# Performance work log

Measured on AMD Instinct MI355X. Metric: run time of the kernel, lower is better.

## Reference

```python
import jax, jax.numpy as jnp
import numpy as np

D_MODEL, D_K, D_V, D_H, SEQ = 1024, 64, 64, 16, 4096


def setup_inputs() -> dict:
    key = jax.random.key(0)
    ks = jax.random.split(key, 16)
    s = lambda fan_in: 1.0 / np.sqrt(fan_in)
    return {
        "X": jax.random.normal(ks[0], (SEQ, D_MODEL), jnp.float32),
        # shared Q/K/V projections (nn.Linear stores weight as [out, in])
        "Wq": jax.random.uniform(ks[1], (D_K, D_MODEL), jnp.float32, -s(D_MODEL), s(D_MODEL)),
        "bq": jax.random.uniform(ks[2], (D_K,), jnp.float32, -s(D_MODEL), s(D_MODEL)),
        "Wk": jax.random.uniform(ks[3], (D_K, D_MODEL), jnp.float32, -s(D_MODEL), s(D_MODEL)),
        "bk": jax.random.uniform(ks[4], (D_K,), jnp.float32, -s(D_MODEL), s(D_MODEL)),
        "Wv": jax.random.uniform(ks[5], (D_V, D_MODEL), jnp.float32, -s(D_MODEL), s(D_MODEL)),
        "bv": jax.random.uniform(ks[6], (D_V,), jnp.float32, -s(D_MODEL), s(D_MODEL)),
        # per-head linears stacked along head axis
        "Whq": jax.random.uniform(ks[7], (D_H, D_K, D_K), jnp.float32, -s(D_K), s(D_K)),
        "bhq": jax.random.uniform(ks[8], (D_H, D_K), jnp.float32, -s(D_K), s(D_K)),
        "Whk": jax.random.uniform(ks[9], (D_H, D_K, D_K), jnp.float32, -s(D_K), s(D_K)),
        "bhk": jax.random.uniform(ks[10], (D_H, D_K), jnp.float32, -s(D_K), s(D_K)),
        "Whv": jax.random.uniform(ks[11], (D_H, D_V, D_V), jnp.float32, -s(D_V), s(D_V)),
        "bhv": jax.random.uniform(ks[12], (D_H, D_V), jnp.float32, -s(D_V), s(D_V)),
        # final projection: d_h*d_v -> d_model
        "Wo": jax.random.uniform(ks[13], (D_MODEL, D_H * D_V), jnp.float32, -s(D_H * D_V), s(D_H * D_V)),
        "bo": jax.random.uniform(ks[14], (D_MODEL,), jnp.float32, -s(D_H * D_V), s(D_H * D_V)),
    }


def reference(X, Wq, bq, Wk, bk, Wv, bv, Whq, bhq, Whk, bhk, Whv, bhv, Wo, bo):
    # shared projections: [T, d_k] / [T, d_v]
    Q = X @ Wq.T + bq
    K = X @ Wk.T + bk
    V = X @ Wv.T + bv
    # per-head linears, all heads at once: [H, T, d_k]
    qh = jnp.einsum("tk,hjk->htj", Q, Whq) + bhq[:, None, :]
    kh = jnp.einsum("tk,hjk->htj", K, Whk) + bhk[:, None, :]
    vh = jnp.einsum("tv,hjv->htj", V, Whv) + bhv[:, None, :]
    # scaled dot-product attention per head: [H, T, T]
    scale = 1.0 / jnp.sqrt(jnp.asarray(Q.shape[-1], X.dtype))
    attn = jax.nn.softmax(jnp.einsum("htk,hsk->hts", qh, kh) * scale, axis=-1)
    rep = jnp.einsum("hts,hsv->htv", attn, vh)  # [H, T, d_v]
    # hstack heads -> [T, H*d_v], then final projection
    concat = rep.transpose(1, 0, 2).reshape(X.shape[0], -1)
    return concat @ Wo.T + bo
```

## Files before the change

### kernel.cpp

```cpp
#include <hip/hip_runtime.h>

#define T 4096
#define DM 1024
#define DK 64
#define H 16

typedef short s8 __attribute__((ext_vector_type(8)));
typedef float f4 __attribute__((ext_vector_type(4)));
typedef float f16v __attribute__((ext_vector_type(16)));
typedef unsigned short us4 __attribute__((ext_vector_type(4)));
typedef unsigned u32x2 __attribute__((ext_vector_type(2)));
typedef unsigned u32x4 __attribute__((ext_vector_type(4)));
typedef __bf16 bf2 __attribute__((ext_vector_type(2)));

#define MFMA16(a,b,c) __builtin_amdgcn_mfma_f32_16x16x32_bf16((a),(b),(c),0,0,0)
#define MFMA32(a,b,c) __builtin_amdgcn_mfma_f32_32x32x16_bf16((a),(b),(c),0,0,0)
#define SCALE_Q 0.18033688011112042f

__device__ __forceinline__ unsigned short f2bf(float x){
  __bf16 b = (__bf16)x;
  return __builtin_bit_cast(unsigned short, b);
}
__device__ __forceinline__ unsigned pk2(float a, float b){
  bf2 v; v[0] = (__bf16)a; v[1] = (__bf16)b;
  return __builtin_bit_cast(unsigned, v);
}

__device__ __forceinline__ void gload16(const void* g, void* lds){
  __builtin_amdgcn_global_load_lds((const __attribute__((address_space(1))) unsigned int*)g,
                                   (__attribute__((address_space(3))) unsigned int*)lds,
                                   16, 0, 0);
}

__device__ __forceinline__ void swp(unsigned X, unsigned Y, unsigned &E, unsigned &O){
#if __has_builtin(__builtin_amdgcn_permlane32_swap)
  auto a = __builtin_amdgcn_permlane32_swap(X, Y, false, false);
  E = a[0]; O = a[1];
#else
  int l = threadIdx.x & 63;
  unsigned sx = __builtin_amdgcn_ds_bpermute(((l & 31) << 2), X);
  unsigned sy = __builtin_amdgcn_ds_bpermute(((l & 31) << 2), Y);
  unsigned hx = __builtin_amdgcn_ds_bpermute((((l & 31) + 32) << 2), X);
  unsigned hy = __builtin_amdgcn_ds_bpermute((((l & 31) + 32) << 2), Y);
  E = (l < 32) ? sx : sy;
  O = (l < 32) ? hx : hy;
#endif
}

__global__ void cvt_bf16(const float* __restrict__ in, unsigned short* __restrict__ out, int n4){
  int i = blockIdx.x * blockDim.x + threadIdx.x;
  if (i >= n4) return;
  float4 v = reinterpret_cast<const float4*>(in)[i];
  us4 o;
  o[0] = f2bf(v.x); o[1] = f2bf(v.y); o[2] = f2bf(v.z); o[3] = f2bf(v.w);
  reinterpret_cast<us4*>(out)[i] = o;
}

#define N_WOB (DM * DM / 4)
#define N_W3  (64 * DM / 4)
#define N_WH  (16 * 64 * 64 / 4)
__global__ __launch_bounds__(256) void prep_all(
    const float* __restrict__ Wo,
    const float* __restrict__ Wq, const float* __restrict__ Wk, const float* __restrict__ Wv,
    const float* __restrict__ Whq, const float* __restrict__ Whk, const float* __restrict__ Whv,
    const float* __restrict__ bq, const float* __restrict__ bk, const float* __restrict__ bv,
    const float* __restrict__ bhq, const float* __restrict__ bhk, const float* __restrict__ bhv,
    unsigned short* __restrict__ Wob, unsigned short* __restrict__ W3b,
    unsigned short* __restrict__ Whb, float* __restrict__ beff){
  int idx = blockIdx.x * 256 + threadIdx.x;
  if (idx < N_WOB){
    float4 v = reinterpret_cast<const float4*>(Wo)[idx];
    us4 o; o[0]=f2bf(v.x); o[1]=f2bf(v.y); o[2]=f2bf(v.z); o[3]=f2bf(v.w);
    reinterpret_cast<us4*>(Wob)[idx] = o;
    return;
  }
  idx -= N_WOB;
  if (idx < 3 * N_W3){
    int seg = idx / N_W3, i = idx - seg * N_W3;
    const float* src = (seg == 0) ? Wq : ((seg == 1) ? Wk : Wv);
    float4 v = reinterpret_cast<const float4*>(src)[i];
    us4 o; o[0]=f2bf(v.x); o[1]=f2bf(v.y); o[2]=f2bf(v.z); o[3]=f2bf(v.w);
    reinterpret_cast<us4*>(W3b)[seg * N_W3 + i] = o;
    return;
  }
  idx -= 3 * N_W3;
  if (idx < 3 * N_WH){
    int seg = idx / N_WH, i = idx - seg * N_WH;
    const float* src = (seg == 0) ? Whq : ((seg == 1) ? Whk : Whv);
    float s = (seg == 0) ? SCALE_Q : 1.0f;
    float4 v = reinterpret_cast<const float4*>(src)[i];
    us4 o; o[0]=f2bf(v.x*s); o[1]=f2bf(v.y*s); o[2]=f2bf(v.z*s); o[3]=f2bf(v.w*s);
    reinterpret_cast<us4*>(Whb)[seg * N_WH + i] = o;
    return;
  }
  idx -= 3 * N_WH;
  if (idx < 3072){
    int seg = idx >> 10, j = idx & 1023;
    const float* Wh = (seg == 0) ? Whq : ((seg == 1) ? Whk : Whv);
    const float* b  = (seg == 0) ? bq  : ((seg == 1) ? bk  : bv);
    const float* bh = (seg == 0) ? bhq : ((seg == 1) ? bhk : bhv);
    float s = (seg == 0) ? SCALE_Q : 1.0f;
    const float* wr = Wh + j * 64;
    float acc = 0.f;
    #pragma unroll 8
    for (int k = 0; k < 64; ++k) acc += wr[k] * b[k];
    beff[idx] = (acc + bh[j]) * s;
  }
}

template<int MODE, int BM, int BN, int NT>
__global__ __launch_bounds__(256) void gemmX(const unsigned short* __restrict__ A,
                       const unsigned short* __restrict__ B,
                       const float* __restrict__ bias,
                       unsigned short* __restrict__ q_out,
                       unsigned short* __restrict__ k_out,
                       unsigned short* __restrict__ v_out,
                       float* __restrict__ f_out){
  __shared__ __align__(16) short la[2][BM * 64];
  __shared__ __align__(16) short lb[2][BN * 64];
  const int tid = threadIdx.x;
  const int wv = tid >> 6, l = tid & 63;
  const int lr = l & 15, lh = l >> 4;
  const int wr = wv >> 1, wc = wv & 1;
  const int tm = blockIdx.x / NT, tn = blockIdx.x % NT;
  const int t0 = tm * BM, o0 = tn * BN;
  constexpr int MF = BM / 32;
  constexpr int NF = BN / 32;
  constexpr int ACH = BM / 32;
  constexpr int BCH = BN / 32;
  constexpr int LAB = BM * 128;
  constexpr int LBB = BN * 128;

  f4 acc[MF][NF];
  #pragma unroll
  for (int i = 0; i < MF; ++i)
    #pragma unroll
    for (int j = 0; j < NF; ++j) acc[i][j] = (f4){0.f, 0.f, 0.f, 0.f};

  const int srow = tid >> 3;
  const int scs  = (tid & 7) ^ (srow & 7);
  const unsigned short* ap = A + (size_t)(t0 + srow) * DM + scs * 8;
  const unsigned short* bp = B + (size_t)(o0 + srow) * DM + scs * 8;
  char* ad = (char*)&la[0][0] + tid * 16;
  char* bd = (char*)&lb[0][0] + tid * 16;

  auto stage = [&](int BUF){
    #pragma unroll
    for (int i = 0; i < ACH; ++i)
      gload16(ap + (size_t)i * 32 * DM, ad + BUF * LAB + i * 4096);
    #pragma unroll
    for (int i = 0; i < BCH; ++i)
      gload16(bp + (size_t)i * 32 * DM, bd + BUF * LBB + i * 4096);
    ap += 64; bp += 64;
  };

  const int asw0 = (lh ^ (lr & 7)) * 16, asw1 = ((lh ^ 4) ^ (lr & 7)) * 16;
  const char* aB0 = (const char*)&la[0][0] + (wr * (BM / 2) + lr) * 128 + asw0;
  const char* aB1 = (const char*)&la[0][0] + (wr * (BM / 2) + lr) * 128 + asw1;
  const char* bB0 = (const char*)&lb[0][0] + (wc * (BN / 2) + lr) * 128 + asw0;
  const char* bB1 = (const char*)&lb[0][0] + (wc * (BN / 2) + lr) * 128 + asw1;

  auto step = [&](int BUF, bool dostage){
    if (dostage) stage(BUF ^ 1);
    s8 af[MF][2], bfr[NF][2];
    #pragma unroll
    for (int mf = 0; mf < MF; ++mf){
      af[mf][0] = *(const s8*)(aB0 + BUF * LAB + mf * 2048);
      af[mf][1] = *(const s8*)(aB1 + BUF * LAB + mf * 2048);
    }
    #pragma unroll
    for (int nf = 0; nf < NF; ++nf){
      bfr[nf][0] = *(const s8*)(bB0 + BUF * LBB + nf * 2048);
      bfr[nf][1] = *(const s8*)(bB1 + BUF * LBB + nf * 2048);
    }
    __builtin_amdgcn_s_setprio(1);
    #pragma unroll
    for (int mf = 0; mf < MF; ++mf)
      #pragma unroll
      for (int nf = 0; nf < NF; ++nf){
        acc[mf][nf] = MFMA16(af[mf][0], bfr[nf][0], acc[mf][nf]);
        acc[mf][nf] = MFMA16(af[mf][1], bfr[nf][1], acc[mf][nf]);
      }
    __builtin_amdgcn_s_setprio(0);
    __syncthreads();
  };

  stage(0);
  __syncthreads();
  #pragma unroll 1
  for (int t2 = 0; t2 < 8; ++t2){
    step(0, true);
    step(1, t2 < 7);
  }

  #pragma unroll
  for (int nf = 0; nf < NF; ++nf){
    int o = o0 + wc * (BN / 2) + nf * 16 + lr;
    float bs = (MODE == 4) ? 0.f : bias[o];
    int sel = o >> 6, oc = o & 63;
    unsigned short* yo = (sel == 0) ? q_out : ((sel == 1) ? k_out : v_out);
    #pragma unroll
    for (int mf = 0; mf < MF; ++mf)
      #pragma unroll
      for (int r = 0; r < 4; ++r){
        int t = t0 + wr * (BM / 2) + mf * 16 + lh * 4 + r;
        float v = acc[mf][nf][r] + bs;
        if (MODE == 2) f_out[(size_t)t * DM + o] = v;
        else           yo[(size_t)t * 64 + oc] = f2bf(v);
      }
  }
}

__global__ __launch_bounds__(256) void gemm_heads(const unsigned short* __restrict__ Yq,
                        const unsigned short* __restrict__ Yk,
                        const unsigned short* __restrict__ Yv,
                        const unsigned short* __restrict__ Whb,
                        const float* __restrict__ beff,
                        unsigned short* __restrict__ qhb,
                        unsigned short* __restrict__ khb,
                        unsigned short* __restrict__ vtb){
  const int tid = threadIdx.x;
  const int wv = tid >> 6, l = tid & 63;
  const int lr = l & 15, lh = l >> 4;
  const int rem = blockIdx.x % 48, tb = blockIdx.x / 48;
  const int kind = rem >> 4, h = rem & 15;
  const unsigned short* Y = (kind == 0) ? Yq : ((kind == 1) ? Yk : Yv);
  const unsigned short* B = Whb + (size_t)rem * 4096;
  const int t0 = tb * 256 + wv * 64;

  s8 wf[4][2], yf[4][2];
  #pragma unroll
  for (int nf = 0; nf < 4; ++nf)
    #pragma unroll
    for (int hf = 0; hf < 2; ++hf)
      wf[nf][hf] = *reinterpret_cast<const s8*>(B + (size_t)(nf * 16 + lr) * 64 + hf * 32 + lh * 8);
  #pragma unroll
  for (int mf = 0; mf < 4; ++mf)
    #pragma unroll
    for (int hf = 0; hf < 2; ++hf)
      yf[mf][hf] = *reinterpret_cast<const s8*>(Y + (size_t)(t0 + mf * 16 + lr) * 64 + hf * 32 + lh * 8);

  f4 acc[4][4];
  #pragma unroll
  for (int i = 0; i < 4; ++i)
    #pragma unroll
    for (int j = 0; j < 4; ++j) acc[i][j] = (f4){0.f, 0.f, 0.f, 0.f};

  if (kind < 2){
    #pragma unroll
    for (int mf = 0; mf < 4; ++mf)
      #pragma unroll
      for (int nf = 0; nf < 4; ++nf){
        acc[mf][nf] = MFMA16(yf[mf][0], wf[nf][0], acc[mf][nf]);
        acc[mf][nf] = MFMA16(yf[mf][1], wf[nf][1], acc[mf][nf]);
      }
    unsigned short* out = (kind == 0) ? qhb : khb;
    #pragma unroll
    for (int nf = 0; nf < 4; ++nf){
      int j = nf * 16 + lr;
      float bs = beff[rem * 64 + j];
      #pragma unroll
      for (int mf = 0; mf < 4; ++mf)
        #pragma unroll
        for (int r = 0; r < 4; ++r){
          int t = t0 + mf * 16 + lh * 4 + r;
          out[((size_t)h * T + t) * DK + j] = f2bf(acc[mf][nf][r] + bs);
        }
    }
  } else {
    #pragma unroll
    for (int nf = 0; nf < 4; ++nf)
      #pragma unroll
      for (int mf = 0; mf < 4; ++mf){
        acc[nf][mf] = MFMA16(wf[nf][0], yf[mf][0], acc[nf][mf]);
        acc[nf][mf] = MFMA16(wf[nf][1], yf[mf][1], acc[nf][mf]);
      }
    #pragma unroll
    for (int nf = 0; nf < 4; ++nf){
      float4 bsv = *reinterpret_cast<const float4*>(beff + rem * 64 + nf * 16 + lh * 4);
      #pragma unroll
      for (int r = 0; r < 4; ++r){
        int j = nf * 16 + lh * 4 + r;
        float bs = (r == 0) ? bsv.x : ((r == 1) ? bsv.y : ((r == 2) ? bsv.z : bsv.w));
        #pragma unroll
        for (int mf = 0; mf < 4; ++mf){
          int t = t0 + mf * 16 + lr;
          vtb[((size_t)h * DK + j) * T + t] = f2bf(acc[nf][mf][r] + bs);
        }
      }
    }
  }
}

__global__ __launch_bounds__(128) void attn_fwd(const unsigned short* __restrict__ qh,
                         const unsigned short* __restrict__ kh,
                         const unsigned short* __restrict__ vt,
                         unsigned short* __restrict__ cat){
  __shared__ __align__(16) char ldsb[2][16384];
  const int tid = threadIdx.x;
  const int wv = tid >> 6, l = tid & 63;
  const int l31 = l & 31, h5 = l >> 5, l7 = l & 7;
  const int h = blockIdx.x >> 5, qblk = blockIdx.x & 31;
  const int Qw = qblk * 128 + wv * 64;

  s8 qf[2][4];
  #pragma unroll
  for (int qt = 0; qt < 2; ++qt)
    #pragma unroll
    for (int kk = 0; kk < 4; ++kk)
      qf[qt][kk] = *reinterpret_cast<const s8*>(
          qh + ((size_t)h * T + Qw + qt * 32 + l31) * DK + kk * 16 + h5 * 8);

  float ls[2] = {0.f, 0.f};
  f16v oa[2][2];
  #pragma unroll
  for (int qt = 0; qt < 2; ++qt)
    #pragma unroll
    for (int dt = 0; dt < 2; ++dt)
      #pragma unroll
      for (int i = 0; i < 16; ++i) oa[qt][dt][i] = 0.f;

  const int srow = tid >> 3;
  const int scs  = (tid & 7) ^ (srow & 7);
  const unsigned short* kp = kh + (size_t)h * T * DK + srow * DK + scs * 8;
  const unsigned short* vp = vt + (size_t)h * DK * T + srow * T + scs * 8;
  char* sd = &ldsb[0][0] + tid * 16;

  auto stage = [&](int BUF){
    #pragma unroll
    for (int i = 0; i < 4; ++i)
      gload16(kp + (size_t)i * 16 * DK, sd + BUF * 16384 + i * 2048);
    #pragma unroll
    for (int i = 0; i < 4; ++i)
      gload16(vp + (size_t)i * 16 * T, sd + BUF * 16384 + 8192 + i * 2048);
    kp += 64 * DK; vp += 64;
  };

  const char* ba[4];
  #pragma unroll
  for (int kk = 0; kk < 4; ++kk)
    ba[kk] = &ldsb[0][0] + l31 * 128 + ((((kk << 1) | h5) ^ l7) << 4);

  auto step = [&](int BUF, bool dostage){
    if (dostage) stage(BUF ^ 1);
    const int bo = BUF * 16384;
    s8 kf0[4], kf1[4], vf0[4], vf1[4];
    #pragma unroll
    for (int kk = 0; kk < 4; ++kk){
      kf0[kk] = *(const s8*)(ba[kk] + bo);
      kf1[kk] = *(const s8*)(ba[kk] + bo + 4096);
    }
    #pragma unroll
    for (int p = 0; p < 4; ++p){
      vf0[p] = *(const s8*)(ba[p] + bo + 8192);
      vf1[p] = *(const s8*)(ba[p] + bo + 12288);
    }
    #pragma unroll
    for (int qt = 0; qt < 2; ++qt){
      f16v sc0, sc1;
      #pragma unroll
      for (int i = 0; i < 16; ++i){ sc0[i] = 0.f; sc1[i] = 0.f; }
      __builtin_amdgcn_s_setprio(1);
      #pragma unroll
      for (int kk = 0; kk < 4; ++kk) sc0 = MFMA32(kf0[kk], qf[qt][kk], sc0);
      #pragma unroll
      for (int kk = 0; kk < 4; ++kk) sc1 = MFMA32(kf1[kk], qf[qt][kk], sc1);
      __builtin_amdgcn_s_setprio(0);
      float p0[16], p1[16];
      #pragma unroll
      for (int i = 0; i < 16; ++i){
        p0[i] = __builtin_amdgcn_exp2f(sc0[i]);
        p1[i] = __builtin_amdgcn_exp2f(sc1[i]);
      }
      float r0 = (p0[0]+p0[1]) + (p0[2]+p0[3]);
      float r1 = (p0[4]+p0[5]) + (p0[6]+p0[7]);
      float r2 = (p0[8]+p0[9]) + (p0[10]+p0[11]);
      float r3 = (p0[12]+p0[13]) + (p0[14]+p0[15]);
      float r4 = (p1[0]+p1[1]) + (p1[2]+p1[3]);
      float r5 = (p1[4]+p1[5]) + (p1[6]+p1[7]);
      float r6 = (p1[8]+p1[9]) + (p1[10]+p1[11]);
      float r7 = (p1[12]+p1[13]) + (p1[14]+p1[15]);
      ls[qt] += ((r0+r1)+(r2+r3)) + ((r4+r5)+(r6+r7));
      unsigned a0 = pk2(p0[0],p0[1]),  a1 = pk2(p0[2],p0[3]);
      unsigned a2 = pk2(p0[4],p0[5]),  a3 = pk2(p0[6],p0[7]);
      unsigned a4 = pk2(p0[8],p0[9]),  a5 = pk2(p0[10],p0[11]);
      unsigned a6 = pk2(p0[12],p0[13]), a7 = pk2(p0[14],p0[15]);
      unsigned b0 = pk2(p1[0],p1[1]),  b1 = pk2(p1[2],p1[3]);
      unsigned b2 = pk2(p1[4],p1[5]),  b3 = pk2(p1[6],p1[7]);
      unsigned b4 = pk2(p1[8],p1[9]),  b5 = pk2(p1[10],p1[11]);
      unsigned b6 = pk2(p1[12],p1[13]), b7 = pk2(p1[14],p1[15]);
      unsigned e0,o0, e1,o1, e2,o2, e3,o3, e4,o4, e5,o5, e6,o6, e7,o7;
      swp(a0, a2, e0, o0);  swp(a1, a3, e1, o1);
      swp(a4, a6, e2, o2);  swp(a5, a7, e3, o3);
      swp(b0, b2, e4, o4);  swp(b1, b3, e5, o5);
      swp(b4, b6, e6, o6);  swp(b5, b7, e7, o7);
      u32x4 pu0 = {e0, e1, o0, o1};
      u32x4 pu1 = {e2, e3, o2, o3};
      u32x4 pu2 = {e4, e5, o4, o5};
      u32x4 pu3 = {e6, e7, o6, o7};
      s8 pa0 = __builtin_bit_cast(s8, pu0);
      s8 pa1 = __builtin_bit_cast(s8, pu1);
      s8 pa2 = __builtin_bit_cast(s8, pu2);
      s8 pa3 = __builtin_bit_cast(s8, pu3);
      __builtin_amdgcn_s_setprio(1);
      oa[qt][0] = MFMA32(vf0[0], pa0, oa[qt][0]);
      oa[qt][0] = MFMA32(vf0[1], pa1, oa[qt][0]);
      oa[qt][0] = MFMA32(vf0[2], pa2, oa[qt][0]);
      oa[qt][0] = MFMA32(vf0[3], pa3, oa[qt][0]);
      oa[qt][1] = MFMA32(vf1[0], pa0, oa[qt][1]);
      oa[qt][1] = MFMA32(vf1[1], pa1, oa[qt][1]);
      oa[qt][1] = MFMA32(vf1[2], pa2, oa[qt][1]);
      oa[qt][1] = MFMA32(vf1[3], pa3, oa[qt][1]);
      __builtin_amdgcn_s_setprio(0);
    }
    __syncthreads();
  };

  stage(0);
  __syncthreads();
  #pragma unroll 1
  for (int it = 0; it < 32; ++it){
    step(0, true);
    step(1, it < 31);
  }

  #pragma unroll
  for (int qt = 0; qt < 2; ++qt){
    float lq = ls[qt] + __shfl_xor(ls[qt], 32);
    float inv = 1.f / lq;
    const int t = Qw + qt * 32 + l31;
    unsigned short* crow = cat + (size_t)t * DM + h * DK;
    #pragma unroll
    for (int g = 0; g < 4; ++g){
      u32x2 w0, w1;
      w0[0] = pk2(oa[qt][0][g*4+0] * inv, oa[qt][0][g*4+1] * inv);
      w0[1] = pk2(oa[qt][0][g*4+2] * inv, oa[qt][0][g*4+3] * inv);
      w1[0] = pk2(oa[qt][1][g*4+0] * inv, oa[qt][1][g*4+1] * inv);
      w1[1] = pk2(oa[qt][1][g*4+2] * inv, oa[qt][1][g*4+3] * inv);
      *reinterpret_cast<u32x2*>(crow + g * 8 + h5 * 4)      = w0;
      *reinterpret_cast<u32x2*>(crow + 32 + g * 8 + h5 * 4) = w1;
    }
  }
}

extern "C" void kernel_launch(void* const* d_in, const int* in_sizes, int n_in,
                              void* d_out, int out_size, void* d_ws, size_t ws_size,
                              hipStream_t stream){
  const float* X   = (const float*)d_in[0];
  const float* Wq  = (const float*)d_in[1];
  const float* bq  = (const float*)d_in[2];
  const float* Wk  = (const float*)d_in[3];
  const float* bk  = (const float*)d_in[4];
  const float* Wv  = (const float*)d_in[5];
  const float* bv  = (const float*)d_in[6];
  const float* Whq = (const float*)d_in[7];
  const float* bhq = (const float*)d_in[8];
  const float* Whk = (const float*)d_in[9];
  const float* bhk = (const float*)d_in[10];
  const float* Whv = (const float*)d_in[11];
  const float* bhv = (const float*)d_in[12];
  const float* Wo  = (const float*)d_in[13];
  const float* bo  = (const float*)d_in[14];

  char* w = (char*)d_ws;
  size_t off = 0;
  auto alloc = [&](size_t bytes) -> char* {
    char* p = w + off;
    off = (off + bytes + 255) & ~(size_t)255;
    return p;
  };
  unsigned short* Xbf = (unsigned short*)alloc((size_t)T * DM * 2);
  unsigned short* Wob = (unsigned short*)alloc((size_t)DM * DM * 2);
  unsigned short* W3b = (unsigned short*)alloc((size_t)192 * DM * 2);
  unsigned short* Whb = (unsigned short*)alloc((size_t)48 * 64 * 64 * 2);
  float* beff = (float*)alloc(48 * 64 * 4);
  unsigned short* Yq  = (unsigned short*)alloc((size_t)T * 64 * 2);
  unsigned short* Yk  = (unsigned short*)alloc((size_t)T * 64 * 2);
  unsigned short* Yv  = (unsigned short*)alloc((size_t)T * 64 * 2);
  unsigned short* qhb = (unsigned short*)alloc((size_t)H * T * DK * 2);
  unsigned short* khb = (unsigned short*)alloc((size_t)H * T * DK * 2);
  unsigned short* vtb = (unsigned short*)alloc((size_t)H * T * DK * 2);
  unsigned short* cat = Xbf;

  cvt_bf16<<<(T * DM / 4) / 256, 256, 0, stream>>>(X, Xbf, T * DM / 4);
  {
    int total = N_WOB + 3 * N_W3 + 3 * N_WH + 3072;
    prep_all<<<(total + 255) / 256, 256, 0, stream>>>(
        Wo, Wq, Wk, Wv, Whq, Whk, Whv, bq, bk, bv, bhq, bhk, bhv,
        Wob, W3b, Whb, beff);
  }

  gemmX<4, 64, 64, 3><<<(T / 64) * 3, 256, 0, stream>>>(Xbf, W3b, nullptr, Yq, Yk, Yv, nullptr);

  gemm_heads<<<(T / 256) * 48, 256, 0, stream>>>(Yq, Yk, Yv, Whb, beff, qhb, khb, vtb);

  attn_fwd<<<(T / 128) * H, 128, 0, stream>>>(qhb, khb, vtb, cat);

  gemmX<2, 128, 64, 16><<<(T / 128) * 16, 256, 0, stream>>>(cat, Wob, bo, nullptr, nullptr, nullptr, (float*)d_out);
}
```

Before: 142.9 us.

## Split attention KV tiles across wave pairs with LDS reduction of partial outputs

The attention kernel now runs 4 waves per block instead of 2. Each query half is handled by two waves that each process half of every 64-key tile, which halves per-wave MFMA, exp and register work per step. Partial output accumulators and row sums are combined through LDS at the end. This raises the number of resident waves to hide latency and spreads global staging over more threads, at the cost of a final LDS reduction and extra barrier participants.

```diff
diff --git a/kernel.cpp b/kernel.cpp
--- a/kernel.cpp
+++ b/kernel.cpp
@@ -292,16 +292,18 @@
   }
 }
 
-__global__ __launch_bounds__(128) void attn_fwd(const unsigned short* __restrict__ qh,
+__global__ __launch_bounds__(256) void attn_fwd(const unsigned short* __restrict__ qh,
                          const unsigned short* __restrict__ kh,
                          const unsigned short* __restrict__ vt,
                          unsigned short* __restrict__ cat){
   __shared__ __align__(16) char ldsb[2][16384];
+  __shared__ float lred[2][64][2];
   const int tid = threadIdx.x;
   const int wv = tid >> 6, l = tid & 63;
   const int l31 = l & 31, h5 = l >> 5, l7 = l & 7;
+  const int qh_ = wv & 1, kvh = wv >> 1;
   const int h = blockIdx.x >> 5, qblk = blockIdx.x & 31;
-  const int Qw = qblk * 128 + wv * 64;
+  const int Q0w = qblk * 128 + qh_ * 64;
 
   s8 qf[2][4];
   #pragma unroll
@@ -309,7 +311,7 @@
     #pragma unroll
     for (int kk = 0; kk < 4; ++kk)
       qf[qt][kk] = *reinterpret_cast<const s8*>(
-          qh + ((size_t)h * T + Qw + qt * 32 + l31) * DK + kk * 16 + h5 * 8);
+          qh + ((size_t)h * T + Q0w + qt * 32 + l31) * DK + kk * 16 + h5 * 8);
 
   float ls[2] = {0.f, 0.f};
   f16v oa[2][2];
@@ -327,90 +329,69 @@
   char* sd = &ldsb[0][0] + tid * 16;
 
   auto stage = [&](int BUF){
-    #pragma unroll
-    for (int i = 0; i < 4; ++i)
-      gload16(kp + (size_t)i * 16 * DK, sd + BUF * 16384 + i * 2048);
-    #pragma unroll
-    for (int i = 0; i < 4; ++i)
-      gload16(vp + (size_t)i * 16 * T, sd + BUF * 16384 + 8192 + i * 2048);
+    gload16(kp,           sd + BUF * 16384);
+    gload16(kp + 32 * DK, sd + BUF * 16384 + 4096);
+    gload16(vp,           sd + BUF * 16384 + 8192);
+    gload16(vp + 32 * T,  sd + BUF * 16384 + 12288);
     kp += 64 * DK; vp += 64;
   };
 
-  const char* ba[4];
+  const char* kb[4];
   #pragma unroll
   for (int kk = 0; kk < 4; ++kk)
-    ba[kk] = &ldsb[0][0] + l31 * 128 + ((((kk << 1) | h5) ^ l7) << 4);
+    kb[kk] = &ldsb[0][0] + (kvh * 32 + l31) * 128 + ((((kk << 1) | h5) ^ l7) << 4);
+  const char* vb[2][2];
+  #pragma unroll
+  for (int dt = 0; dt < 2; ++dt)
+    #pragma unroll
+    for (int ks = 0; ks < 2; ++ks)
+      vb[dt][ks] = &ldsb[0][0] + 8192 + (dt * 32 + l31) * 128 +
+                   (((kvh * 4 + (ks << 1) + h5) ^ l7) << 4);
 
   auto step = [&](int BUF, bool dostage){
     if (dostage) stage(BUF ^ 1);
     const int bo = BUF * 16384;
-    s8 kf0[4], kf1[4], vf0[4], vf1[4];
-    #pragma unroll
-    for (int kk = 0; kk < 4; ++kk){
-      kf0[kk] = *(const s8*)(ba[kk] + bo);
-      kf1[kk] = *(const s8*)(ba[kk] + bo + 4096);
-    }
-    #pragma unroll
-    for (int p = 0; p < 4; ++p){
-      vf0[p] = *(const s8*)(ba[p] + bo + 8192);
-      vf1[p] = *(const s8*)(ba[p] + bo + 12288);
-    }
+    s8 kf[4], vf[2][2];
+    #pragma unroll
+    for (int kk = 0; kk < 4; ++kk) kf[kk] = *(const s8*)(kb[kk] + bo);
+    #pragma unroll
+    for (int dt = 0; dt < 2; ++dt)
+      #pragma unroll
+      for (int ks = 0; ks < 2; ++ks) vf[dt][ks] = *(const s8*)(vb[dt][ks] + bo);
+
     #pragma unroll
     for (int qt = 0; qt < 2; ++qt){
-      f16v sc0, sc1;
-      #pragma unroll
-      for (int i = 0; i < 16; ++i){ sc0[i] = 0.f; sc1[i] = 0.f; }
+      f16v sc;
+      #pragma unroll
+      for (int i = 0; i < 16; ++i) sc[i] = 0.f;
       __builtin_amdgcn_s_setprio(1);
       #pragma unroll
-      for (int kk = 0; kk < 4; ++kk) sc0 = MFMA32(kf0[kk], qf[qt][kk], sc0);
-      #pragma unroll
-      for (int kk = 0; kk < 4; ++kk) sc1 = MFMA32(kf1[kk], qf[qt][kk], sc1);
+      for (int kk = 0; kk < 4; ++kk) sc = MFMA32(kf[kk], qf[qt][kk], sc);
       __builtin_amdgcn_s_setprio(0);
-      float p0[16], p1[16];
-      #pragma unroll
-      for (int i = 0; i < 16; ++i){
-        p0[i] = __builtin_amdgcn_exp2f(sc0[i]);
-        p1[i] = __builtin_amdgcn_exp2f(sc1[i]);
-      }
-      float r0 = (p0[0]+p0[1]) + (p0[2]+p0[3]);
-      float r1 = (p0[4]+p0[5]) + (p0[6]+p0[7]);
-      float r2 = (p0[8]+p0[9]) + (p0[10]+p0[11]);
-      float r3 = (p0[12]+p0[13]) + (p0[14]+p0[15]);
-      float r4 = (p1[0]+p1[1]) + (p1[2]+p1[3]);
-      float r5 = (p1[4]+p1[5]) + (p1[6]+p1[7]);
-      float r6 = (p1[8]+p1[9]) + (p1[10]+p1[11]);
-      float r7 = (p1[12]+p1[13]) + (p1[14]+p1[15]);
-      ls[qt] += ((r0+r1)+(r2+r3)) + ((r4+r5)+(r6+r7));
-      unsigned a0 = pk2(p0[0],p0[1]),  a1 = pk2(p0[2],p0[3]);
-      unsigned a2 = pk2(p0[4],p0[5]),  a3 = pk2(p0[6],p0[7]);
-      unsigned a4 = pk2(p0[8],p0[9]),  a5 = pk2(p0[10],p0[11]);
-      unsigned a6 = pk2(p0[12],p0[13]), a7 = pk2(p0[14],p0[15]);
-      unsigned b0 = pk2(p1[0],p1[1]),  b1 = pk2(p1[2],p1[3]);
-      unsigned b2 = pk2(p1[4],p1[5]),  b3 = pk2(p1[6],p1[7]);
-      unsigned b4 = pk2(p1[8],p1[9]),  b5 = pk2(p1[10],p1[11]);
-      unsigned b6 = pk2(p1[12],p1[13]), b7 = pk2(p1[14],p1[15]);
-      unsigned e0,o0, e1,o1, e2,o2, e3,o3, e4,o4, e5,o5, e6,o6, e7,o7;
+      float p[16];
+      #pragma unroll
+      for (int i = 0; i < 16; ++i) p[i] = __builtin_amdgcn_exp2f(sc[i]);
+      float r0 = (p[0]+p[1]) + (p[2]+p[3]);
+      float r1 = (p[4]+p[5]) + (p[6]+p[7]);
+      float r2 = (p[8]+p[9]) + (p[10]+p[11]);
+      float r3 = (p[12]+p[13]) + (p[14]+p[15]);
+      ls[qt] += (r0+r1) + (r2+r3);
+      unsigned a0 = pk2(p[0],p[1]),  a1 = pk2(p[2],p[3]);
+      unsigned a2 = pk2(p[4],p[5]),  a3 = pk2(p[6],p[7]);
+      unsigned a4 = pk2(p[8],p[9]),  a5 = pk2(p[10],p[11]);
+      unsigned a6 = pk2(p[12],p[13]), a7 = pk2(p[14],p[15]);
+      unsigned e0,o0, e1,o1, e2,o2, e3,o3;
       swp(a0, a2, e0, o0);  swp(a1, a3, e1, o1);
       swp(a4, a6, e2, o2);  swp(a5, a7, e3, o3);
-      swp(b0, b2, e4, o4);  swp(b1, b3, e5, o5);
-      swp(b4, b6, e6, o6);  swp(b5, b7, e7, o7);
       u32x4 pu0 = {e0, e1, o0, o1};
       u32x4 pu1 = {e2, e3, o2, o3};
-      u32x4 pu2 = {e4, e5, o4, o5};
-      u32x4 pu3 = {e6, e7, o6, o7};
       s8 pa0 = __builtin_bit_cast(s8, pu0);
       s8 pa1 = __builtin_bit_cast(s8, pu1);
-      s8 pa2 = __builtin_bit_cast(s8, pu2);
-      s8 pa3 = __builtin_bit_cast(s8, pu3);
       __builtin_amdgcn_s_setprio(1);
-      oa[qt][0] = MFMA32(vf0[0], pa0, oa[qt][0]);
-      oa[qt][0] = MFMA32(vf0[1], pa1, oa[qt][0]);
-      oa[qt][0] = MFMA32(vf0[2], pa2, oa[qt][0]);
-      oa[qt][0] = MFMA32(vf0[3], pa3, oa[qt][0]);
-      oa[qt][1] = MFMA32(vf1[0], pa0, oa[qt][1]);
-      oa[qt][1] = MFMA32(vf1[1], pa1, oa[qt][1]);
-      oa[qt][1] = MFMA32(vf1[2], pa2, oa[qt][1]);
-      oa[qt][1] = MFMA32(vf1[3], pa3, oa[qt][1]);
+      oa[qt][0] = MFMA32(vf[0][0], pa0, oa[qt][0]);
+      oa[qt][0] = MFMA32(vf[0][1], pa1, oa[qt][0]);
+      oa[qt][1] = MFMA32(vf[1][0], pa0, oa[qt][1]);
+      oa[qt][1] = MFMA32(vf[1][1], pa1, oa[qt][1]);
       __builtin_amdgcn_s_setprio(0);
     }
     __syncthreads();
@@ -424,21 +405,52 @@
     step(1, it < 31);
   }
 
-  #pragma unroll
-  for (int qt = 0; qt < 2; ++qt){
-    float lq = ls[qt] + __shfl_xor(ls[qt], 32);
-    float inv = 1.f / lq;
-    const int t = Qw + qt * 32 + l31;
-    unsigned short* crow = cat + (size_t)t * DM + h * DK;
-    #pragma unroll
-    for (int g = 0; g < 4; ++g){
-      u32x2 w0, w1;
-      w0[0] = pk2(oa[qt][0][g*4+0] * inv, oa[qt][0][g*4+1] * inv);
-      w0[1] = pk2(oa[qt][0][g*4+2] * inv, oa[qt][0][g*4+3] * inv);
-      w1[0] = pk2(oa[qt][1][g*4+0] * inv, oa[qt][1][g*4+1] * inv);
-      w1[1] = pk2(oa[qt][1][g*4+2] * inv, oa[qt][1][g*4+3] * inv);
-      *reinterpret_cast<u32x2*>(crow + g * 8 + h5 * 4)      = w0;
-      *reinterpret_cast<u32x2*>(crow + 32 + g * 8 + h5 * 4) = w1;
+  float* red = (float*)&ldsb[0][0];
+  if (kvh == 1){
+    #pragma unroll
+    for (int qt = 0; qt < 2; ++qt){
+      lred[qh_][l][qt] = ls[qt];
+      #pragma unroll
+      for (int dt = 0; dt < 2; ++dt){
+        float* dst = red + qh_ * 4096 + (qt * 2 + dt) * 1024 + l * 16;
+        #pragma unroll
+        for (int g = 0; g < 4; ++g){
+          f4 v = {oa[qt][dt][g*4+0], oa[qt][dt][g*4+1],
+                  oa[qt][dt][g*4+2], oa[qt][dt][g*4+3]};
+          *reinterpret_cast<f4*>(dst + g * 4) = v;
+        }
+      }
+    }
+  }
+  __syncthreads();
+  if (kvh == 0){
+    #pragma unroll
+    for (int qt = 0; qt < 2; ++qt){
+      float lqp = ls[qt] + lred[qh_][l][qt];
+      float lq = lqp + __shfl_xor(lqp, 32);
+      float inv = 1.f / lq;
+      const int t = Q0w + qt * 32 + l31;
+      unsigned short* crow = cat + (size_t)t * DM + h * DK;
+      #pragma unroll
+      for (int dt = 0; dt < 2; ++dt){
+        const float* src = red + qh_ * 4096 + (qt * 2 + dt) * 1024 + l * 16;
+        f16v osum;
+        #pragma unroll
+        for (int g = 0; g < 4; ++g){
+          f4 v = *reinterpret_cast<const f4*>(src + g * 4);
+          osum[g*4+0] = oa[qt][dt][g*4+0] + v[0];
+          osum[g*4+1] = oa[qt][dt][g*4+1] + v[1];
+          osum[g*4+2] = oa[qt][dt][g*4+2] + v[2];
+          osum[g*4+3] = oa[qt][dt][g*4+3] + v[3];
+        }
+        #pragma unroll
+        for (int g = 0; g < 4; ++g){
+          u32x2 w;
+          w[0] = pk2(osum[g*4+0] * inv, osum[g*4+1] * inv);
+          w[1] = pk2(osum[g*4+2] * inv, osum[g*4+3] * inv);
+          *reinterpret_cast<u32x2*>(crow + dt * 32 + g * 8 + h5 * 4) = w;
+        }
+      }
     }
   }
 }
@@ -494,7 +506,7 @@
 
   gemm_heads<<<(T / 256) * 48, 256, 0, stream>>>(Yq, Yk, Yv, Whb, beff, qhb, khb, vtb);
 
-  attn_fwd<<<(T / 128) * H, 128, 0, stream>>>(qhb, khb, vtb, cat);
+  attn_fwd<<<(T / 128) * H, 256, 0, stream>>>(qhb, khb, vtb, cat);
 
   gemmX<2, 128, 64, 16><<<(T / 128) * 16, 256, 0, stream>>>(cat, Wob, bo, nullptr, nullptr, nullptr, (float*)d_out);
 }
```

New measurement: 143.2 us. No clear change (+0.2%).
